# Optimization experiments

Measured on AMD Instinct MI355X. Metric: run time of the kernel, lower is better.

The kernel has to match this reference:

```python
import jax, jax.numpy as jnp
import numpy as np

IN_DIM = 64
OUT_DIM = 64
NUM_HEADS = 4
NEG_SLOPE = 0.2
GAMMA = 1.0  # constraint_gamma
NUM_VARS = 100000
NUM_CLAUSES = 100000
NUM_CLUSTERS = 2048
VARS_PER = 64
CLAUSES_PER = 64
NUM_EDGES = 400000


def _xavier(k, shape):
    bound = np.sqrt(6.0 / (shape[0] + shape[1])).astype(np.float32)
    return jax.random.uniform(k, shape, jnp.float32, -bound, bound)


def setup_inputs() -> dict:
    key = jax.random.key(0)
    ks = jax.random.split(key, 11)
    return {
        "x_var": jax.random.normal(ks[0], (NUM_VARS, IN_DIM), jnp.float32),
        "x_clause": jax.random.normal(ks[1], (NUM_CLAUSES, IN_DIM), jnp.float32),
        "var_clause_edge_index": jax.random.randint(ks[2], (2, NUM_EDGES), 0, NUM_VARS),
        "edge_polarity": jax.random.normal(ks[3], (NUM_EDGES, 1), jnp.float32),
        "cluster_var_ids": jax.random.randint(ks[4], (NUM_CLUSTERS, VARS_PER), 0, NUM_VARS),
        "cluster_clause_ids": jax.random.randint(ks[5], (NUM_CLUSTERS, CLAUSES_PER), 0, NUM_CLAUSES),
        "satisfaction_scores": jax.random.uniform(ks[6], (NUM_CLAUSES,), jnp.float32),
        "active_heads": 4,
        "W_Q": _xavier(ks[7], (OUT_DIM, IN_DIM)),
        "W_K": _xavier(ks[8], (OUT_DIM, IN_DIM)),
        "W_V": _xavier(ks[9], (OUT_DIM, IN_DIM)),
        "head_weights": jnp.ones((NUM_HEADS,), jnp.float32),
        "out_proj_w": _xavier(ks[10], (OUT_DIM, OUT_DIM)),
        "out_proj_b": jnp.zeros((OUT_DIM,), jnp.float32),
    }


def reference(x_var, x_clause, var_clause_edge_index, edge_polarity,
              cluster_var_ids, cluster_clause_ids, satisfaction_scores,
              active_heads, W_Q, W_K, W_V, head_weights, out_proj_w, out_proj_b):
    # NOTE: var_clause_edge_index / edge_polarity are accepted but unused,
    # matching the original forward body.
    num_vars = x_var.shape[0]
    x_all = jnp.concatenate([x_var, x_clause], axis=0)            # [N, D]
    Q = x_all @ W_Q.T
    K = x_all @ W_K.T
    V = x_all @ W_V.T

    # Block-diagonal cluster layout: [C, S] with S = VARS_PER + CLAUSES_PER
    nodes = jnp.concatenate([cluster_var_ids, cluster_clause_ids + num_vars], axis=1)
    Qc = Q[nodes]                                                 # [C, S, D]
    Kc = K[nodes]
    Vc = V[nodes]

    scale = jnp.asarray(np.sqrt(OUT_DIM), Qc.dtype)
    scores = jnp.einsum('csd,ctd->cst', Qc, Kc) / scale            # [C, S, S]
    # constraint-aware bias on clause columns (added before leaky_relu)
    bias = jnp.concatenate(
        [jnp.zeros(cluster_var_ids.shape, scores.dtype),
         GAMMA * satisfaction_scores[cluster_clause_ids]], axis=1)  # [C, S]
    scores = jax.nn.leaky_relu(scores + bias[:, None, :], NEG_SLOPE)
    attn = jax.nn.softmax(scores, axis=-1)

    head_w = jnp.mean(head_weights[:active_heads])
    h = jnp.einsum('cst,ctd->csd', attn, Vc) * head_w             # [C, S, D]

    flat = nodes.reshape(-1)
    out = jnp.zeros_like(x_all).at[flat].add(h.reshape(-1, OUT_DIM))
    count = jnp.zeros((x_all.shape[0],), x_all.dtype).at[flat].add(1.0)
    out = out / jnp.maximum(count, 1.0)[:, None]
    out = out @ out_proj_w.T + out_proj_b

    return (x_var + out[:num_vars], x_clause + out[num_vars:])
```

## Files before the change

### kernel.cpp

```cpp
#include <hip/hip_runtime.h>


#define NV 100000
#define NN 200000
#define NCLUST 2048
#define XS 72

typedef __attribute__((ext_vector_type(8))) short short8;
typedef __attribute__((ext_vector_type(16))) float floatx16;

__device__ __forceinline__ unsigned short f2bf(float f) {
    union { float f; unsigned u; } v; v.f = f;
    unsigned r = v.u + 0x7fffu + ((v.u >> 16) & 1u);
    return (unsigned short)(r >> 16);
}
__device__ __forceinline__ int crow(int r, int lane) {
    return (r & 3) + 8 * (r >> 2) + 4 * (lane >> 5);
}

__global__ __launch_bounds__(256) void prep_kernel(
    const float* __restrict__ WQ, const float* __restrict__ WK,
    const float* __restrict__ WV, const float* __restrict__ Wout,
    const float* __restrict__ head_weights, const int* __restrict__ active_heads_p,
    unsigned short* __restrict__ Mtr, unsigned short* __restrict__ Pbf)
{
    int o = blockIdx.x * blockDim.x + threadIdx.x;
    int ah = active_heads_p[0];
    float hw = 0.f;
    for (int i = 0; i < ah; ++i) hw += head_weights[i];
    hw /= (float)ah;
    if (o < 4096) {
        int d = o >> 6, a = o & 63;
        float acc = 0.f;
        for (int j = 0; j < 64; ++j) acc += WQ[j*64 + a] * WK[j*64 + d];
        Mtr[o] = f2bf(acc * 0.125f);
    } else if (o < 8192) {
        int o2 = o - 4096;
        int j = o2 >> 6, b = o2 & 63;
        float acc = 0.f;
        for (int d = 0; d < 64; ++d) acc += Wout[j*64 + d] * WV[d*64 + b];
        Pbf[o2] = f2bf(acc * hw);
    }
}

__global__ __launch_bounds__(256, 4) void attn_kernel(
    const float* __restrict__ x_var, const float* __restrict__ x_clause,
    const int* __restrict__ cvar, const int* __restrict__ ccl,
    const float* __restrict__ sat, const unsigned short* __restrict__ Mtr,
    unsigned short* __restrict__ accum_bf, float* __restrict__ countv)
{
    __shared__ unsigned short Xc[128 * XS];
    __shared__ unsigned short Eh[128 * XS];
    __shared__ int   ids[128];
    __shared__ float biascl[64];

    const int tid = threadIdx.x, lane = tid & 63, w = tid >> 6;
    const int c = blockIdx.x;
    const int m = lane & 31, hk = (lane >> 5) * 8;

    {
        const int r = tid >> 1, half = tid & 1;
        int nid;
        const float* src;
        if (r < 64) {
            nid = cvar[c * 64 + r];
            src = x_var + (size_t)nid * 64;
        } else {
            int cid = ccl[c * 64 + (r - 64)];
            nid = NV + cid;
            src = x_clause + (size_t)cid * 64;
            if (half) biascl[r - 64] = sat[cid];
        }
        if (!half) ids[r] = nid;
        union { unsigned short us[32]; short8 v[4]; } hb;
        const float4* s4 = (const float4*)src + half * 8;
        #pragma unroll
        for (int i = 0; i < 8; ++i) {
            float4 v = s4[i];
            hb.us[i*4+0] = f2bf(v.x); hb.us[i*4+1] = f2bf(v.y);
            hb.us[i*4+2] = f2bf(v.z); hb.us[i*4+3] = f2bf(v.w);
        }
        const int c0 = half * 32;
        #pragma unroll
        for (int i = 0; i < 4; ++i) *(short8*)&Xc[r * XS + c0 + i * 8] = hb.v[i];
    }
    __syncthreads();
    if (tid < 128) atomicAdd(&countv[ids[tid]], 1.0f);

    {
        floatx16 z0 = {}, z1 = {};
        #pragma unroll
        for (int ks = 0; ks < 4; ++ks) {
            short8 mb0 = *(const short8*)(Mtr + m * 64 + ks * 16 + hk);
            short8 mb1 = *(const short8*)(Mtr + (32 + m) * 64 + ks * 16 + hk);
            short8 a = *(const short8*)&Xc[(w * 32 + m) * XS + ks * 16 + hk];
            z0 = __builtin_amdgcn_mfma_f32_32x32x16_bf16(a, mb0, z0, 0, 0, 0);
            z1 = __builtin_amdgcn_mfma_f32_32x32x16_bf16(a, mb1, z1, 0, 0, 0);
        }
        #pragma unroll
        for (int r = 0; r < 16; ++r) {
            int row = w * 32 + crow(r, lane);
            Eh[row * XS + m]      = f2bf(z0[r]);
            Eh[row * XS + 32 + m] = f2bf(z1[r]);
        }
    }

    floatx16 sc[4] = {{}, {}, {}, {}};
    #pragma unroll
    for (int ks = 0; ks < 4; ++ks) {
        short8 a = *(const short8*)&Eh[(w * 32 + m) * XS + ks * 16 + hk];
        #pragma unroll
        for (int nt = 0; nt < 4; ++nt) {
            short8 b = *(const short8*)&Xc[(nt * 32 + m) * XS + ks * 16 + hk];
            sc[nt] = __builtin_amdgcn_mfma_f32_32x32x16_bf16(a, b, sc[nt], 0, 0, 0);
        }
    }

    const float b2 = biascl[m], b3 = biascl[32 + m];
    #pragma unroll
    for (int r = 0; r < 16; ++r) {
        float a0 = sc[0][r], a1 = sc[1][r], a2 = sc[2][r] + b2, a3 = sc[3][r] + b3;
        a0 = a0 > 0.f ? a0 : 0.2f * a0;
        a1 = a1 > 0.f ? a1 : 0.2f * a1;
        a2 = a2 > 0.f ? a2 : 0.2f * a2;
        a3 = a3 > 0.f ? a3 : 0.2f * a3;
        a0 = __expf(a0); a1 = __expf(a1); a2 = __expf(a2); a3 = __expf(a3);
        float s4 = (a0 + a1) + (a2 + a3);
        #pragma unroll
        for (int off = 1; off < 32; off <<= 1) s4 += __shfl_xor(s4, off, 64);
        float inv = __builtin_amdgcn_rcpf(s4);
        sc[0][r] = a0 * inv; sc[1][r] = a1 * inv;
        sc[2][r] = a2 * inv; sc[3][r] = a3 * inv;
    }

    #pragma unroll
    for (int r = 0; r < 16; ++r) {
        int row = w * 32 + crow(r, lane);
        Eh[row * XS + m]      = f2bf(sc[0][r]);
        Eh[row * XS + 32 + m] = f2bf(sc[1][r]);
    }

    floatx16 g0 = {}, g1 = {};
    #pragma unroll
    for (int ks = 0; ks < 4; ++ks) {
        short8 a = *(const short8*)&Eh[(w * 32 + m) * XS + ks * 16 + hk];
        short8 b0, b1;
        #pragma unroll
        for (int j = 0; j < 8; ++j) {
            int t = ks * 16 + hk + j;
            b0[j] = (short)Xc[t * XS + m];
            b1[j] = (short)Xc[t * XS + 32 + m];
        }
        g0 = __builtin_amdgcn_mfma_f32_32x32x16_bf16(a, b0, g0, 0, 0, 0);
        g1 = __builtin_amdgcn_mfma_f32_32x32x16_bf16(a, b1, g1, 0, 0, 0);
    }

    #pragma unroll
    for (int r = 0; r < 16; ++r) {
        int row = w * 32 + crow(r, lane);
        Eh[row * XS + m]      = f2bf(sc[2][r]);
        Eh[row * XS + 32 + m] = f2bf(sc[3][r]);
    }

    #pragma unroll
    for (int ks = 0; ks < 4; ++ks) {
        short8 a = *(const short8*)&Eh[(w * 32 + m) * XS + ks * 16 + hk];
        short8 b0, b1;
        #pragma unroll
        for (int j = 0; j < 8; ++j) {
            int t = 64 + ks * 16 + hk + j;
            b0[j] = (short)Xc[t * XS + m];
            b1[j] = (short)Xc[t * XS + 32 + m];
        }
        g0 = __builtin_amdgcn_mfma_f32_32x32x16_bf16(a, b0, g0, 0, 0, 0);
        g1 = __builtin_amdgcn_mfma_f32_32x32x16_bf16(a, b1, g1, 0, 0, 0);
    }

    const bool ev = !(lane & 1);
    const int colbase = ev ? m : (31 + m);
    #pragma unroll
    for (int r = 0; r < 16; ++r) {
        int row = w * 32 + crow(r, lane);
        int nid = ids[row];
        float a0 = g0[r], a1 = g1[r];
        float t0 = __shfl_xor(a0, 1, 64);
        float t1 = __shfl_xor(a1, 1, 64);
        float lo = ev ? a0 : t1;
        float hi = ev ? t0 : a1;
        unsigned pk = (unsigned)f2bf(lo) | ((unsigned)f2bf(hi) << 16);
        unsigned long long addr =
            (unsigned long long)(accum_bf + (size_t)nid * 64 + colbase);
        asm volatile("global_atomic_pk_add_bf16 %0, %1, off"
                     :: "v"(addr), "v"(pk) : "memory");
    }
}

__global__ __launch_bounds__(256, 4) void finalize_kernel(
    const float* __restrict__ x_var, const float* __restrict__ x_clause,
    const unsigned short* __restrict__ accum_bf, const float* __restrict__ countv,
    const unsigned short* __restrict__ Pbf, const float* __restrict__ bout,
    float* __restrict__ out)
{
    __shared__ float cnts[256];
    const int tid = threadIdx.x, lane = tid & 63, w = tid >> 6;
    const int base = blockIdx.x * 256;
    {
        int n = base + tid;
        cnts[tid] = (n < NN) ? countv[n] : 1.f;
    }
    __syncthreads();

    const int m = lane & 31, hk = (lane >> 5) * 8;
    short8 pb[2][4];
    #pragma unroll
    for (int nt = 0; nt < 2; ++nt)
        #pragma unroll
        for (int ks = 0; ks < 4; ++ks)
            pb[nt][ks] = *(const short8*)(Pbf + (nt * 32 + m) * 64 + ks * 16 + hk);
    const float bias0 = bout[m], bias1 = bout[32 + m];

    #pragma unroll
    for (int tm = 0; tm < 2; ++tm) {
        int mt = w * 2 + tm;
        const unsigned short* arow = accum_bf + (size_t)(base + mt * 32 + m) * 64;
        floatx16 c0 = {}, c1 = {};
        #pragma unroll
        for (int ks = 0; ks < 4; ++ks) {
            short8 a = *(const short8*)(arow + ks * 16 + hk);
            c0 = __builtin_amdgcn_mfma_f32_32x32x16_bf16(a, pb[0][ks], c0, 0, 0, 0);
            c1 = __builtin_amdgcn_mfma_f32_32x32x16_bf16(a, pb[1][ks], c1, 0, 0, 0);
        }
        #pragma unroll
        for (int r = 0; r < 16; ++r) {
            int lrow = mt * 32 + crow(r, lane);
            int n = base + lrow;
            if (n < NN) {
                float inv = 1.0f / fmaxf(cnts[lrow], 1.0f);
                const float* xs = (n < NV) ? (x_var + (size_t)n * 64)
                                           : (x_clause + (size_t)(n - NV) * 64);
                out[(size_t)n * 64 + m]      = xs[m]      + c0[r] * inv + bias0;
                out[(size_t)n * 64 + 32 + m] = xs[32 + m] + c1[r] * inv + bias1;
            }
        }
    }
}

extern "C" void kernel_launch(void* const* d_in, const int* in_sizes, int n_in,
                              void* d_out, int out_size, void* d_ws, size_t ws_size,
                              hipStream_t stream)
{
    const float* x_var        = (const float*)d_in[0];
    const float* x_clause     = (const float*)d_in[1];
    const int*   cvar         = (const int*)d_in[4];
    const int*   ccl          = (const int*)d_in[5];
    const float* sat          = (const float*)d_in[6];
    const int*   active_heads = (const int*)d_in[7];
    const float* WQ           = (const float*)d_in[8];
    const float* WK           = (const float*)d_in[9];
    const float* WV           = (const float*)d_in[10];
    const float* head_weights = (const float*)d_in[11];
    const float* Wout         = (const float*)d_in[12];
    const float* bout         = (const float*)d_in[13];

    unsigned short* accum_bf = (unsigned short*)d_ws;
    float* countv = (float*)(accum_bf + (size_t)NN * 64);
    unsigned short* Mtr = (unsigned short*)(countv + NN);
    unsigned short* Pbf = Mtr + 4096;

    hipMemsetAsync(accum_bf, 0, (size_t)NN * 64 * 2 + (size_t)NN * 4, stream);
    prep_kernel<<<32, 256, 0, stream>>>(WQ, WK, WV, Wout, head_weights, active_heads, Mtr, Pbf);
    attn_kernel<<<NCLUST, 256, 0, stream>>>(x_var, x_clause, cvar, ccl, sat, Mtr, accum_bf, countv);
    finalize_kernel<<<(NN + 255) / 256, 256, 0, stream>>>(x_var, x_clause, accum_bf, countv, Pbf, bout, (float*)d_out);
}
```

Baseline: 213.9 us.

## Process two clusters per attention block with prefetched second-cluster gather

```diff
diff --git a/kernel.cpp b/kernel.cpp
--- a/kernel.cpp
+++ b/kernel.cpp
@@ -7,12 +7,19 @@
 #define XS 72
 
 typedef __attribute__((ext_vector_type(8))) short short8;
+typedef __attribute__((ext_vector_type(4))) unsigned uint4v;
 typedef __attribute__((ext_vector_type(16))) float floatx16;
 
 __device__ __forceinline__ unsigned short f2bf(float f) {
     union { float f; unsigned u; } v; v.f = f;
     unsigned r = v.u + 0x7fffu + ((v.u >> 16) & 1u);
     return (unsigned short)(r >> 16);
+}
+__device__ __forceinline__ unsigned pack2bf(float lo, float hi) {
+    union { float f; unsigned u; } a, b; a.f = lo; b.f = hi;
+    unsigned ra = a.u + 0x7fffu + ((a.u >> 16) & 1u);
+    unsigned rb = b.u + 0x7fffu + ((b.u >> 16) & 1u);
+    return (ra >> 16) | (rb & 0xffff0000u);
 }
 __device__ __forceinline__ int crow(int r, int lane) {
     return (r & 3) + 8 * (r >> 2) + 4 * (lane >> 5);
@@ -43,50 +50,13 @@
     }
 }
 
-__global__ __launch_bounds__(256, 4) void attn_kernel(
-    const float* __restrict__ x_var, const float* __restrict__ x_clause,
-    const int* __restrict__ cvar, const int* __restrict__ ccl,
-    const float* __restrict__ sat, const unsigned short* __restrict__ Mtr,
-    unsigned short* __restrict__ accum_bf, float* __restrict__ countv)
-{
-    __shared__ unsigned short Xc[128 * XS];
-    __shared__ unsigned short Eh[128 * XS];
-    __shared__ int   ids[128];
-    __shared__ float biascl[64];
-
-    const int tid = threadIdx.x, lane = tid & 63, w = tid >> 6;
-    const int c = blockIdx.x;
-    const int m = lane & 31, hk = (lane >> 5) * 8;
-
-    {
-        const int r = tid >> 1, half = tid & 1;
-        int nid;
-        const float* src;
-        if (r < 64) {
-            nid = cvar[c * 64 + r];
-            src = x_var + (size_t)nid * 64;
-        } else {
-            int cid = ccl[c * 64 + (r - 64)];
-            nid = NV + cid;
-            src = x_clause + (size_t)cid * 64;
-            if (half) biascl[r - 64] = sat[cid];
-        }
-        if (!half) ids[r] = nid;
-        union { unsigned short us[32]; short8 v[4]; } hb;
-        const float4* s4 = (const float4*)src + half * 8;
-        #pragma unroll
-        for (int i = 0; i < 8; ++i) {
-            float4 v = s4[i];
-            hb.us[i*4+0] = f2bf(v.x); hb.us[i*4+1] = f2bf(v.y);
-            hb.us[i*4+2] = f2bf(v.z); hb.us[i*4+3] = f2bf(v.w);
-        }
-        const int c0 = half * 32;
-        #pragma unroll
-        for (int i = 0; i < 4; ++i) *(short8*)&Xc[r * XS + c0 + i * 8] = hb.v[i];
-    }
-    __syncthreads();
-    if (tid < 128) atomicAdd(&countv[ids[tid]], 1.0f);
-
+__device__ __forceinline__ void cluster_compute(
+    unsigned short* Xc, unsigned short* Eh,
+    const int* ids, const float* biascl,
+    const unsigned short* __restrict__ Mtr,
+    unsigned short* __restrict__ accum_bf,
+    int lane, int w, int m, int hk)
+{
     {
         floatx16 z0 = {}, z1 = {};
         #pragma unroll
@@ -195,16 +165,100 @@
     }
 }
 
+__global__ __launch_bounds__(256, 3) void attn_kernel(
+    const float* __restrict__ x_var, const float* __restrict__ x_clause,
+    const int* __restrict__ cvar, const int* __restrict__ ccl,
+    const float* __restrict__ sat, const unsigned short* __restrict__ Mtr,
+    unsigned short* __restrict__ accum_bf, float* __restrict__ countv)
+{
+    __shared__ unsigned short Xc[128 * XS];
+    __shared__ unsigned short Eh[128 * XS];
+    __shared__ unsigned stage4[16 * 256];
+    __shared__ int   ids[128];
+    __shared__ float biascl[64];
+
+    const int tid = threadIdx.x, lane = tid & 63, w = tid >> 6;
+    const int m = lane & 31, hk = (lane >> 5) * 8;
+    const int c0 = blockIdx.x * 2;
+    const int r = tid >> 1, half = tid & 1;
+
+    int nid0, nid1;
+    const float *src0, *src1;
+    float satv0 = 0.f, satv1 = 0.f;
+    if (r < 64) {
+        nid0 = cvar[c0 * 64 + r];
+        nid1 = cvar[c0 * 64 + 64 + r];
+        src0 = x_var + (size_t)nid0 * 64;
+        src1 = x_var + (size_t)nid1 * 64;
+    } else {
+        int cid0 = ccl[c0 * 64 + (r - 64)];
+        int cid1 = ccl[c0 * 64 + r];
+        nid0 = NV + cid0; nid1 = NV + cid1;
+        src0 = x_clause + (size_t)cid0 * 64;
+        src1 = x_clause + (size_t)cid1 * 64;
+        if (half) { satv0 = sat[cid0]; satv1 = sat[cid1]; }
+    }
+
+    const float4* s40 = (const float4*)src0 + half * 8;
+    const float4* s41 = (const float4*)src1 + half * 8;
+    float4 v0[8], v1[8];
+    #pragma unroll
+    for (int i = 0; i < 8; ++i) v0[i] = s40[i];
+    #pragma unroll
+    for (int i = 0; i < 8; ++i) v1[i] = s41[i];
+
+    if (!half) atomicAdd(&countv[nid0], 1.0f);
+
+    {
+        union { unsigned u[16]; short8 v[4]; } hb;
+        #pragma unroll
+        for (int i = 0; i < 8; ++i) {
+            hb.u[2*i]   = pack2bf(v0[i].x, v0[i].y);
+            hb.u[2*i+1] = pack2bf(v0[i].z, v0[i].w);
+        }
+        const int cb = half * 32;
+        #pragma unroll
+        for (int i = 0; i < 4; ++i) *(short8*)&Xc[r * XS + cb + i * 8] = hb.v[i];
+    }
+    #pragma unroll
+    for (int i = 0; i < 8; ++i) {
+        stage4[(2*i)   * 256 + tid] = pack2bf(v1[i].x, v1[i].y);
+        stage4[(2*i+1) * 256 + tid] = pack2bf(v1[i].z, v1[i].w);
+    }
+    if (!half) ids[r] = nid0;
+    if (r >= 64 && half) biascl[r - 64] = satv0;
+    __syncthreads();
+
+    cluster_compute(Xc, Eh, ids, biascl, Mtr, accum_bf, lane, w, m, hk);
+    __syncthreads();
+
+    {
+        const int cb = half * 32;
+        #pragma unroll
+        for (int j = 0; j < 4; ++j) {
+            uint4v t;
+            #pragma unroll
+            for (int q = 0; q < 4; ++q) t[q] = stage4[(4*j + q) * 256 + tid];
+            *(uint4v*)&Xc[r * XS + cb + 8 * j] = t;
+        }
+    }
+    if (!half) { ids[r] = nid1; atomicAdd(&countv[nid1], 1.0f); }
+    if (r >= 64 && half) biascl[r - 64] = satv1;
+    __syncthreads();
+
+    cluster_compute(Xc, Eh, ids, biascl, Mtr, accum_bf, lane, w, m, hk);
+}
+
 __global__ __launch_bounds__(256, 4) void finalize_kernel(
     const float* __restrict__ x_var, const float* __restrict__ x_clause,
     const unsigned short* __restrict__ accum_bf, const float* __restrict__ countv,
     const unsigned short* __restrict__ Pbf, const float* __restrict__ bout,
     float* __restrict__ out)
 {
-    __shared__ float cnts[256];
+    __shared__ float cnts[128];
     const int tid = threadIdx.x, lane = tid & 63, w = tid >> 6;
-    const int base = blockIdx.x * 256;
-    {
+    const int base = blockIdx.x * 128;
+    if (tid < 128) {
         int n = base + tid;
         cnts[tid] = (n < NN) ? countv[n] : 1.f;
     }
@@ -219,28 +273,24 @@
             pb[nt][ks] = *(const short8*)(Pbf + (nt * 32 + m) * 64 + ks * 16 + hk);
     const float bias0 = bout[m], bias1 = bout[32 + m];
 
-    #pragma unroll
-    for (int tm = 0; tm < 2; ++tm) {
-        int mt = w * 2 + tm;
-        const unsigned short* arow = accum_bf + (size_t)(base + mt * 32 + m) * 64;
-        floatx16 c0 = {}, c1 = {};
-        #pragma unroll
-        for (int ks = 0; ks < 4; ++ks) {
-            short8 a = *(const short8*)(arow + ks * 16 + hk);
-            c0 = __builtin_amdgcn_mfma_f32_32x32x16_bf16(a, pb[0][ks], c0, 0, 0, 0);
-            c1 = __builtin_amdgcn_mfma_f32_32x32x16_bf16(a, pb[1][ks], c1, 0, 0, 0);
-        }
-        #pragma unroll
-        for (int r = 0; r < 16; ++r) {
-            int lrow = mt * 32 + crow(r, lane);
-            int n = base + lrow;
-            if (n < NN) {
-                float inv = 1.0f / fmaxf(cnts[lrow], 1.0f);
-                const float* xs = (n < NV) ? (x_var + (size_t)n * 64)
-                                           : (x_clause + (size_t)(n - NV) * 64);
-                out[(size_t)n * 64 + m]      = xs[m]      + c0[r] * inv + bias0;
-                out[(size_t)n * 64 + 32 + m] = xs[32 + m] + c1[r] * inv + bias1;
-            }
+    const unsigned short* arow = accum_bf + (size_t)(base + w * 32 + m) * 64;
+    floatx16 c0 = {}, c1 = {};
+    #pragma unroll
+    for (int ks = 0; ks < 4; ++ks) {
+        short8 a = *(const short8*)(arow + ks * 16 + hk);
+        c0 = __builtin_amdgcn_mfma_f32_32x32x16_bf16(a, pb[0][ks], c0, 0, 0, 0);
+        c1 = __builtin_amdgcn_mfma_f32_32x32x16_bf16(a, pb[1][ks], c1, 0, 0, 0);
+    }
+    #pragma unroll
+    for (int r = 0; r < 16; ++r) {
+        int lrow = w * 32 + crow(r, lane);
+        int n = base + lrow;
+        if (n < NN) {
+            float inv = 1.0f / fmaxf(cnts[lrow], 1.0f);
+            const float* xs = (n < NV) ? (x_var + (size_t)n * 64)
+                                       : (x_clause + (size_t)(n - NV) * 64);
+            out[(size_t)n * 64 + m]      = xs[m]      + c0[r] * inv + bias0;
+            out[(size_t)n * 64 + 32 + m] = xs[32 + m] + c1[r] * inv + bias1;
         }
     }
 }
@@ -269,6 +319,6 @@
 
     hipMemsetAsync(accum_bf, 0, (size_t)NN * 64 * 2 + (size_t)NN * 4, stream);
     prep_kernel<<<32, 256, 0, stream>>>(WQ, WK, WV, Wout, head_weights, active_heads, Mtr, Pbf);
-    attn_kernel<<<NCLUST, 256, 0, stream>>>(x_var, x_clause, cvar, ccl, sat, Mtr, accum_bf, countv);
-    finalize_kernel<<<(NN + 255) / 256, 256, 0, stream>>>(x_var, x_clause, accum_bf, countv, Pbf, bout, (float*)d_out);
-}
+    attn_kernel<<<NCLUST / 2, 256, 0, stream>>>(x_var, x_clause, cvar, ccl, sat, Mtr, accum_bf, countv);
+    finalize_kernel<<<(NN + 127) / 128, 256, 0, stream>>>(x_var, x_clause, accum_bf, countv, Pbf, bout, (float*)d_out);
+}
```

After: 217.5 us. No clear change (+1.6%).
